# Kernel tuning notes

Measured on AMD Instinct MI355X. Metric: run time of the kernel, lower is better.

## Reference

```python
import jax, jax.numpy as jnp
import numpy as np

HEADS = 8
DIM_HEAD = 64
SCALE = DIM_HEAD ** -0.5

def setup_inputs() -> dict:
    key = jax.random.key(0)
    k1, k2, k3 = jax.random.split(key, 3)
    B, N, D = 4, 2048, 512
    inner = HEADS * DIM_HEAD  # 512
    x = jax.random.normal(k1, (B, N, D), dtype=jnp.float32)
    w_qkv = jax.random.normal(k2, (D, inner * 3), dtype=jnp.float32) * (D ** -0.5)
    w_out = jax.random.normal(k3, (inner, D), dtype=jnp.float32) * (inner ** -0.5)
    b_out = jnp.zeros((D,), dtype=jnp.float32)
    return {"x": x, "w_qkv": w_qkv, "w_out": w_out, "b_out": b_out}

def reference(x, w_qkv, w_out, b_out):
    B, N, D = x.shape
    qkv = x @ w_qkv  # [B, N, 3*inner]
    q, k, v = jnp.split(qkv, 3, axis=-1)
    # b n (h d) -> b h n d
    def to_heads(t):
        return t.reshape(B, N, HEADS, DIM_HEAD).transpose(0, 2, 1, 3)
    q, k, v = to_heads(q), to_heads(k), to_heads(v)
    dots = jnp.einsum('bhid,bhjd->bhij', q, k) * SCALE  # [B,H,N,N]
    attn = jax.nn.softmax(dots, axis=-1)
    out = jnp.einsum('bhij,bhjd->bhid', attn, v)  # [B,H,N,Dh]
    out = out.transpose(0, 2, 1, 3).reshape(B, N, HEADS * DIM_HEAD)
    return out @ w_out + b_out
```

## Files before the change

kernel.cpp:

```cpp
#include <hip/hip_runtime.h>
#include <hip/hip_bf16.h>
#include <math.h>
#include <stdint.h>


typedef unsigned short u16;
typedef __attribute__((ext_vector_type(4))) float f32x4;
typedef __attribute__((ext_vector_type(8))) short bf16x8;
typedef __attribute__((ext_vector_type(4))) short s16x4;

#define AS1 __attribute__((address_space(1)))
#define AS3 __attribute__((address_space(3)))
#define MFMA(a, b, c) __builtin_amdgcn_mfma_f32_16x16x32_bf16(a, b, c, 0, 0, 0)
#define QSCALE 0.180336880f

__device__ __forceinline__ u16 f2bf(float f) {
  union { float f; unsigned u; } v; v.f = f;
  unsigned r = v.u + 0x7FFFu + ((v.u >> 16) & 1u);
  return (u16)(r >> 16);
}
__device__ __forceinline__ float bf2f(u16 b) {
  union { unsigned u; float f; } v; v.u = ((unsigned)b) << 16; return v.f;
}
__device__ __forceinline__ void splitbf(float x, u16& hi, u16& lo) {
  hi = f2bf(x); lo = f2bf(x - bf2f(hi));
}
__device__ __forceinline__ void gld16(const u16* g, u16* l) {
  __builtin_amdgcn_global_load_lds((const AS1 void*)g, (AS3 void*)l, 16, 0, 0);
}
__device__ __forceinline__ float u2f(unsigned u) {
  union { unsigned u; float f; } v; v.u = u; return v.f;
}
__device__ __forceinline__ unsigned f2u(float f) {
  union { float f; unsigned u; } v; v.f = f; return v.u;
}
__device__ __forceinline__ int cvtpk(float lo, float hi) {
  int r; asm("v_cvt_pk_bf16_f32 %0, %1, %2" : "=v"(r) : "v"(lo), "v"(hi));
  return r;
}
__device__ __forceinline__ float fexp2(float x) {
  float r; asm("v_exp_f32 %0, %1" : "=v"(r) : "v"(x));
  return r;
}

__global__ void k_cast(const float* __restrict__ s, u16* __restrict__ h, int n) {
  int i = (blockIdx.x * 256 + threadIdx.x) * 4;
  if (i < n) {
    f32x4 v = *(const f32x4*)&s[i];
    s16x4 hh;
    #pragma unroll
    for (int j = 0; j < 4; ++j) hh[j] = (short)f2bf(v[j]);
    *(s16x4*)&h[i] = hh;
  }
}

__global__ void k_tsplit(const float* __restrict__ s, u16* __restrict__ h,
                         u16* __restrict__ l, int N, int total) {
  int i = blockIdx.x * 256 + threadIdx.x;
  if (i < total) {
    int n = i >> 9, k = i & 511;
    u16 a, b; splitbf(s[(size_t)k * N + n], a, b);
    h[i] = a; l[i] = b;
  }
}

template <int TERMS>
__device__ __forceinline__ void gemm_core(
    const u16* __restrict__ Ah,
    const u16* __restrict__ Bh, const u16* __restrict__ Bl,
    char* sm, int rowA, int rowB, int tid, f32x4 (&acc)[4][4]) {
  const int wid = tid >> 6, lane = tid & 63;
  const int x = lane & 15, h = lane >> 4;
  const int wr = wid >> 1, wc = wid & 1;
  const int d0 = wid * 1024 + lane * 16;
  const int lg0 = d0 ^ (((d0 >> 7) & 7) << 4);
  const int srow = lg0 >> 6;
  const int scol = (lg0 & 63) >> 1;
  const int swk = ((lane >> 1) & 7) << 4;
  const char* smA = sm + (((wr * 64 + x) * 64 + h * 16) ^ swk);
  const char* smB = sm + (((wc * 64 + x) * 64 + h * 16) ^ swk);

  for (int kt = 0; kt < 16; ++kt) {
    const int kofs = kt * 32;
    __syncthreads();
    #pragma unroll
    for (int r = 0; r < 2; ++r) {
      const int row  = r * 64 + srow;
      const int ldst = r * 4096 + wid * 1024;
      const size_t ga = (size_t)(rowA + row) * 512 + kofs + scol;
      const size_t gb = (size_t)(rowB + row) * 512 + kofs + scol;
      gld16(Ah + ga, (u16*)(sm + ldst));
      gld16(Bh + gb, (u16*)(sm + 16384 + ldst));
      if (TERMS == 2) gld16(Bl + gb, (u16*)(sm + 24576 + ldst));
    }
    __syncthreads();
    bf16x8 a_h[4], b_h[4], b_l[4];
    #pragma unroll
    for (int i = 0; i < 4; ++i)
      a_h[i] = *(const bf16x8*)(smA + i * 1024);
    #pragma unroll
    for (int j = 0; j < 4; ++j) {
      b_h[j] = *(const bf16x8*)(smB + 16384 + j * 1024);
      if (TERMS == 2) b_l[j] = *(const bf16x8*)(smB + 24576 + j * 1024);
    }
    __builtin_amdgcn_s_setprio(1);
    #pragma unroll
    for (int i = 0; i < 4; ++i)
      #pragma unroll
      for (int j = 0; j < 4; ++j) {
        acc[i][j] = MFMA(a_h[i], b_h[j], acc[i][j]);
        if (TERMS == 2) acc[i][j] = MFMA(a_h[i], b_l[j], acc[i][j]);
      }
    __builtin_amdgcn_s_setprio(0);
  }
}

__global__ __launch_bounds__(256) void k_gemm_qkv(
    const u16* __restrict__ Ah,
    const u16* __restrict__ Bh, const u16* __restrict__ Bl,
    u16* __restrict__ Qb, u16* __restrict__ Kb, u16* __restrict__ Vt) {
  __shared__ __align__(1024) char sm[32768];
  const int tid = threadIdx.x, lane = tid & 63, wid = tid >> 6;
  const int x = lane & 15, h = lane >> 4;
  const int wr = wid >> 1, wc = wid & 1;
  const int rowA = blockIdx.x * 128, rowB = blockIdx.y * 128;
  f32x4 acc[4][4] = {};
  if (rowB >= 1024)
    gemm_core<1>(Ah, Bh, Bl, sm, rowA, rowB, tid, acc);
  else
    gemm_core<2>(Ah, Bh, Bl, sm, rowA, rowB, tid, acc);

  #pragma unroll
  for (int i = 0; i < 4; ++i)
    #pragma unroll
    for (int j = 0; j < 4; ++j) {
      const int n = rowB + wc * 64 + j * 16 + x;
      const int which = n >> 9;
      const int hh = (n >> 6) & 7, d = n & 63;
      const int m0 = rowA + wr * 64 + i * 16 + h * 4;
      const int b = m0 >> 11, is0 = m0 & 2047;
      if (which == 0) {
        #pragma unroll
        for (int r = 0; r < 4; ++r) {
          const size_t idx = ((size_t)((b * 8 + hh) * 2048 + is0 + r)) * 64 + d;
          Qb[idx] = f2bf(acc[i][j][r] * QSCALE);
        }
      } else if (which == 1) {
        #pragma unroll
        for (int r = 0; r < 4; ++r) {
          const size_t idx = ((size_t)((b * 8 + hh) * 2048 + is0 + r)) * 64 + d;
          Kb[idx] = f2bf(acc[i][j][r]);
        }
      } else {
        s16x4 vv;
        #pragma unroll
        for (int r = 0; r < 4; ++r) vv[r] = (short)f2bf(acc[i][j][r]);
        *(s16x4*)&Vt[((size_t)((b * 8 + hh) * 64 + d)) * 2048 + is0] = vv;
      }
    }
}

__global__ __launch_bounds__(256) void k_gemm_out(
    const u16* __restrict__ Ah, const u16* __restrict__ Bh,
    const float* __restrict__ bias, float* __restrict__ out) {
  __shared__ __align__(1024) char sm[32768];
  const int tid = threadIdx.x, lane = tid & 63, wid = tid >> 6;
  const int x = lane & 15, h = lane >> 4;
  const int wr = wid >> 1, wc = wid & 1;
  const int rowA = blockIdx.x * 128, rowB = blockIdx.y * 128;
  f32x4 acc[4][4] = {};
  gemm_core<1>(Ah, Bh, Bh, sm, rowA, rowB, tid, acc);

  #pragma unroll
  for (int i = 0; i < 4; ++i)
    #pragma unroll
    for (int j = 0; j < 4; ++j) {
      const int n = rowB + wc * 64 + j * 16 + x;
      #pragma unroll
      for (int r = 0; r < 4; ++r) {
        const int m = rowA + wr * 64 + i * 16 + h * 4 + r;
        out[(size_t)m * 512 + n] = acc[i][j][r] + bias[n];
      }
    }
}

__global__ __launch_bounds__(128, 2) void k_attn(
    const u16* __restrict__ Qb,
    const u16* __restrict__ Kb, const u16* __restrict__ Vt,
    u16* __restrict__ AO) {
  __shared__ __align__(1024) char sm[40960];
  const int tid = threadIdx.x, wid = tid >> 6, lane = tid & 63;
  const int x = lane & 15, h = lane >> 4;

  const int fid = blockIdx.x;
  const int l = (fid & 7) * 128 + (fid >> 3);
  const int qb = l & 31, bh = l >> 5;

  const size_t base = (size_t)bh * 2048 * 64;
  const int qr0 = qb * 64 + wid * 32;

  bf16x8 qh[2][2];
  #pragma unroll
  for (int g = 0; g < 2; ++g) {
    const size_t rq = base + (size_t)(qr0 + g * 16 + x) * 64 + h * 8;
    #pragma unroll
    for (int ks = 0; ks < 2; ++ks)
      qh[g][ks] = *(const bf16x8*)&Qb[rq + ks * 32];
  }

  bf16x8 ones;
  #pragma unroll
  for (int j = 0; j < 8; ++j) ones[j] = (short)0x3F80;

  int srow[2], scb[2];
  #pragma unroll
  for (int r = 0; r < 2; ++r) {
    const int db = r * 2048 + tid * 16;
    const int lg = db ^ (((db >> 7) & 7) << 4);
    srow[r] = lg >> 6;
    scb[r] = (lg & 63) >> 1;
  }

  const int swk = ((lane >> 1) & 7) << 4;
  const int rdo = (x * 64 + h * 16) ^ swk;
  char* const pb = sm + 32768 + wid * 4096;
  const int pxor = (x & 7) << 4;
  const int prow = x * 128;

  float mrun[2] = {-INFINITY, -INFINITY};
  f32x4 o[2][4] = {};
  f32x4 os[2] = {};

  {
    #pragma unroll
    for (int r = 0; r < 2; ++r) {
      const size_t kR = base + (size_t)srow[r] * 64 + scb[r];
      const size_t vR = base + (size_t)srow[r] * 2048 + scb[r];
      const int db = r * 2048 + tid * 16;
      gld16(Kb + kR,      (u16*)(sm + db));
      gld16(Kb + kR + 32, (u16*)(sm + 4096 + db));
      gld16(Vt + vR,      (u16*)(sm + 8192 + db));
      gld16(Vt + vR + 32, (u16*)(sm + 12288 + db));
    }
  }

  for (int kv = 0; kv < 32; ++kv) {
    const int bb = (kv & 1) * 16384;
    __builtin_amdgcn_s_barrier();
    if (kv < 31) {
      const size_t kvb = (size_t)(kv + 1) * 64;
      char* buf = sm + (16384 - bb);
      #pragma unroll
      for (int r = 0; r < 2; ++r) {
        const size_t kR = base + (kvb + srow[r]) * 64 + scb[r];
        const size_t vR = base + (size_t)srow[r] * 2048 + kvb + scb[r];
        const int db = r * 2048 + tid * 16;
        gld16(Kb + kR,      (u16*)(buf + db));
        gld16(Kb + kR + 32, (u16*)(buf + 4096 + db));
        gld16(Vt + vR,      (u16*)(buf + 8192 + db));
        gld16(Vt + vR + 32, (u16*)(buf + 12288 + db));
      }
      asm volatile("s_waitcnt vmcnt(8)" ::: "memory");
    } else {
      asm volatile("s_waitcnt vmcnt(0)" ::: "memory");
    }
    __builtin_amdgcn_s_barrier();

    const char* smb = sm + bb + rdo;

    f32x4 s[2][4] = {};
    __builtin_amdgcn_s_setprio(1);
    #pragma unroll
    for (int c = 0; c < 4; ++c)
      #pragma unroll
      for (int ks = 0; ks < 2; ++ks) {
        bf16x8 kb_ = *(const bf16x8*)(smb + ks * 4096 + c * 1024);
        s[0][c] = MFMA(kb_, qh[0][ks], s[0][c]);
        s[1][c] = MFMA(kb_, qh[1][ks], s[1][c]);
      }
    __builtin_amdgcn_s_setprio(0);

    float pm[2];
    #pragma unroll
    for (int g = 0; g < 2; ++g) {
      float m0 = fmaxf(fmaxf(s[g][0][0], s[g][0][1]), s[g][0][2]);
      float m1 = fmaxf(fmaxf(s[g][0][3], s[g][1][0]), s[g][1][1]);
      float m2 = fmaxf(fmaxf(s[g][1][2], s[g][1][3]), s[g][2][0]);
      float m3 = fmaxf(fmaxf(s[g][2][1], s[g][2][2]), s[g][2][3]);
      float m4 = fmaxf(fmaxf(s[g][3][0], s[g][3][1]), s[g][3][2]);
      float m5 = fmaxf(fmaxf(m0, m1), m2);
      float p  = fmaxf(fmaxf(fmaxf(m3, m4), s[g][3][3]), m5);
      p = fmaxf(p, __shfl_xor(p, 16, 64));
      p = fmaxf(p, __shfl_xor(p, 32, 64));
      pm[g] = p;
    }

    if (__any((pm[0] > mrun[0] + 7.0f) || (pm[1] > mrun[1] + 7.0f))) {
      #pragma unroll
      for (int g = 0; g < 2; ++g) {
        float mnew = fmaxf(mrun[g], pm[g]);
        float scl = fexp2(mrun[g] - mnew);
        mrun[g] = mnew;
        #pragma unroll
        for (int r = 0; r < 4; ++r) {
          float sq = u2f((unsigned)__builtin_amdgcn_ds_bpermute(
              (20 * h + r) * 4, (int)f2u(scl)));
          os[g][r] *= sq;
          #pragma unroll
          for (int dg = 0; dg < 4; ++dg) o[g][dg][r] *= sq;
        }
      }
    }

    #pragma unroll
    for (int g = 0; g < 2; ++g)
      #pragma unroll
      for (int c = 0; c < 4; ++c) {
        int w0 = cvtpk(fexp2(s[g][c][0] - mrun[g]),
                       fexp2(s[g][c][1] - mrun[g]));
        int w1 = cvtpk(fexp2(s[g][c][2] - mrun[g]),
                       fexp2(s[g][c][3] - mrun[g]));
        int* dst = (int*)(pb + g * 2048 + prow + ((c * 32 + h * 8) ^ pxor));
        dst[0] = w0; dst[1] = w1;
      }

    __builtin_amdgcn_s_setprio(1);
    #pragma unroll
    for (int ch = 0; ch < 2; ++ch) {
      bf16x8 pa0 = *(const bf16x8*)(pb + prow +
                                    ((ch * 64 + h * 16) ^ pxor));
      bf16x8 pa1 = *(const bf16x8*)(pb + 2048 + prow +
                                    ((ch * 64 + h * 16) ^ pxor));
      os[0] = MFMA(pa0, ones, os[0]);
      os[1] = MFMA(pa1, ones, os[1]);
      #pragma unroll
      for (int dg = 0; dg < 4; ++dg) {
        bf16x8 vb = *(const bf16x8*)(smb + 8192 + ch * 4096 + dg * 1024);
        o[0][dg] = MFMA(pa0, vb, o[0][dg]);
        o[1][dg] = MFMA(pa1, vb, o[1][dg]);
      }
    }
    __builtin_amdgcn_s_setprio(0);
  }

  const int b_ = bh >> 3, head = bh & 7;
  #pragma unroll
  for (int g = 0; g < 2; ++g)
    #pragma unroll
    for (int r = 0; r < 4; ++r) {
      const float inv = 1.0f / os[g][r];
      const int row = qr0 + g * 16 + h * 4 + r;
      #pragma unroll
      for (int dg = 0; dg < 4; ++dg) {
        AO[((size_t)(b_ * 2048 + row)) * 512 + head * 64 + dg * 16 + x] =
            f2bf(o[g][dg][r] * inv);
      }
    }
}

extern "C" void kernel_launch(void* const* d_in, const int* in_sizes, int n_in,
                              void* d_out, int out_size, void* d_ws, size_t ws_size,
                              hipStream_t stream) {
  const float* x    = (const float*)d_in[0];
  const float* wqkv = (const float*)d_in[1];
  const float* wout = (const float*)d_in[2];
  const float* bout = (const float*)d_in[3];
  float* out = (float*)d_out;

  char* w = (char*)d_ws;
  u16* xh  = (u16*)(w + 0);
  u16* wqh = (u16*)(w + 16777216);
  u16* wql = (u16*)(w + 18350080);
  u16* woh = (u16*)(w + 19922944);
  u16* wol = (u16*)(w + 20447232);
  u16* Qb  = (u16*)(w + 20971520);
  u16* Kb  = (u16*)(w + 37748736);
  u16* Vt  = (u16*)(w + 46137344);
  u16* AO  = (u16*)(w + 54525952);

  k_cast  <<<4096, 256, 0, stream>>>(x, xh, 4194304);
  k_tsplit<<<3072, 256, 0, stream>>>(wqkv, wqh, wql, 1536, 786432);
  k_tsplit<<<1024, 256, 0, stream>>>(wout, woh, wol, 512, 262144);
  k_gemm_qkv<<<dim3(64, 12), 256, 0, stream>>>(xh, wqh, wql, Qb, Kb, Vt);
  k_attn<<<1024, 128, 0, stream>>>(Qb, Kb, Vt, AO);
  k_gemm_out<<<dim3(64, 4), 256, 0, stream>>>(AO, woh, bout, out);
}
```

Before: 112.1 us.

## Double per-wave query rows in attention kernel to raise K/V reuse

```diff
diff --git a/kernel.cpp b/kernel.cpp
--- a/kernel.cpp
+++ b/kernel.cpp
@@ -188,20 +188,20 @@
     const u16* __restrict__ Qb,
     const u16* __restrict__ Kb, const u16* __restrict__ Vt,
     u16* __restrict__ AO) {
-  __shared__ __align__(1024) char sm[40960];
+  __shared__ __align__(1024) char sm[49152];
   const int tid = threadIdx.x, wid = tid >> 6, lane = tid & 63;
   const int x = lane & 15, h = lane >> 4;
 
   const int fid = blockIdx.x;
-  const int l = (fid & 7) * 128 + (fid >> 3);
-  const int qb = l & 31, bh = l >> 5;
+  const int l = (fid & 7) * 64 + (fid >> 3);
+  const int qb = l & 15, bh = l >> 4;
 
   const size_t base = (size_t)bh * 2048 * 64;
-  const int qr0 = qb * 64 + wid * 32;
-
-  bf16x8 qh[2][2];
-  #pragma unroll
-  for (int g = 0; g < 2; ++g) {
+  const int qr0 = qb * 128 + wid * 64;
+
+  bf16x8 qh[4][2];
+  #pragma unroll
+  for (int g = 0; g < 4; ++g) {
     const size_t rq = base + (size_t)(qr0 + g * 16 + x) * 64 + h * 8;
     #pragma unroll
     for (int ks = 0; ks < 2; ++ks)
@@ -223,13 +223,12 @@
 
   const int swk = ((lane >> 1) & 7) << 4;
   const int rdo = (x * 64 + h * 16) ^ swk;
-  char* const pb = sm + 32768 + wid * 4096;
+  char* const pb = sm + 32768 + wid * 8192;
   const int pxor = (x & 7) << 4;
-  const int prow = x * 128;
-
-  float mrun[2] = {-INFINITY, -INFINITY};
-  f32x4 o[2][4] = {};
-  f32x4 os[2] = {};
+
+  float mrun[4] = {-INFINITY, -INFINITY, -INFINITY, -INFINITY};
+  f32x4 o[4][4] = {};
+  f32x4 os[4] = {};
 
   {
     #pragma unroll
@@ -268,21 +267,22 @@
 
     const char* smb = sm + bb + rdo;
 
-    f32x4 s[2][4] = {};
+    f32x4 s[4][4] = {};
     __builtin_amdgcn_s_setprio(1);
     #pragma unroll
     for (int c = 0; c < 4; ++c)
       #pragma unroll
       for (int ks = 0; ks < 2; ++ks) {
         bf16x8 kb_ = *(const bf16x8*)(smb + ks * 4096 + c * 1024);
-        s[0][c] = MFMA(kb_, qh[0][ks], s[0][c]);
-        s[1][c] = MFMA(kb_, qh[1][ks], s[1][c]);
+        #pragma unroll
+        for (int g = 0; g < 4; ++g)
+          s[g][c] = MFMA(kb_, qh[g][ks], s[g][c]);
       }
     __builtin_amdgcn_s_setprio(0);
 
-    float pm[2];
-    #pragma unroll
-    for (int g = 0; g < 2; ++g) {
+    float pm[4];
+    #pragma unroll
+    for (int g = 0; g < 4; ++g) {
       float m0 = fmaxf(fmaxf(s[g][0][0], s[g][0][1]), s[g][0][2]);
       float m1 = fmaxf(fmaxf(s[g][0][3], s[g][1][0]), s[g][1][1]);
       float m2 = fmaxf(fmaxf(s[g][1][2], s[g][1][3]), s[g][2][0]);
@@ -295,9 +295,10 @@
       pm[g] = p;
     }
 
-    if (__any((pm[0] > mrun[0] + 7.0f) || (pm[1] > mrun[1] + 7.0f))) {
-      #pragma unroll
-      for (int g = 0; g < 2; ++g) {
+    if (__any((pm[0] > mrun[0] + 7.0f) || (pm[1] > mrun[1] + 7.0f) ||
+              (pm[2] > mrun[2] + 7.0f) || (pm[3] > mrun[3] + 7.0f))) {
+      #pragma unroll
+      for (int g = 0; g < 4; ++g) {
         float mnew = fmaxf(mrun[g], pm[g]);
         float scl = fexp2(mrun[g] - mnew);
         mrun[g] = mnew;
@@ -313,31 +314,34 @@
     }
 
     #pragma unroll
-    for (int g = 0; g < 2; ++g)
+    for (int g = 0; g < 4; ++g)
       #pragma unroll
       for (int c = 0; c < 4; ++c) {
         int w0 = cvtpk(fexp2(s[g][c][0] - mrun[g]),
                        fexp2(s[g][c][1] - mrun[g]));
         int w1 = cvtpk(fexp2(s[g][c][2] - mrun[g]),
                        fexp2(s[g][c][3] - mrun[g]));
-        int* dst = (int*)(pb + g * 2048 + prow + ((c * 32 + h * 8) ^ pxor));
+        int* dst = (int*)(pb + (g * 16 + x) * 128 + ((c * 32 + h * 8) ^ pxor));
         dst[0] = w0; dst[1] = w1;
       }
 
     __builtin_amdgcn_s_setprio(1);
     #pragma unroll
     for (int ch = 0; ch < 2; ++ch) {
-      bf16x8 pa0 = *(const bf16x8*)(pb + prow +
-                                    ((ch * 64 + h * 16) ^ pxor));
-      bf16x8 pa1 = *(const bf16x8*)(pb + 2048 + prow +
-                                    ((ch * 64 + h * 16) ^ pxor));
-      os[0] = MFMA(pa0, ones, os[0]);
-      os[1] = MFMA(pa1, ones, os[1]);
+      bf16x8 pa[4];
+      #pragma unroll
+      for (int g = 0; g < 4; ++g)
+        pa[g] = *(const bf16x8*)(pb + (g * 16 + x) * 128 +
+                                 ((ch * 64 + h * 16) ^ pxor));
+      #pragma unroll
+      for (int g = 0; g < 4; ++g)
+        os[g] = MFMA(pa[g], ones, os[g]);
       #pragma unroll
       for (int dg = 0; dg < 4; ++dg) {
         bf16x8 vb = *(const bf16x8*)(smb + 8192 + ch * 4096 + dg * 1024);
-        o[0][dg] = MFMA(pa0, vb, o[0][dg]);
-        o[1][dg] = MFMA(pa1, vb, o[1][dg]);
+        #pragma unroll
+        for (int g = 0; g < 4; ++g)
+          o[g][dg] = MFMA(pa[g], vb, o[g][dg]);
       }
     }
     __builtin_amdgcn_s_setprio(0);
@@ -345,7 +349,7 @@
 
   const int b_ = bh >> 3, head = bh & 7;
   #pragma unroll
-  for (int g = 0; g < 2; ++g)
+  for (int g = 0; g < 4; ++g)
     #pragma unroll
     for (int r = 0; r < 4; ++r) {
       const float inv = 1.0f / os[g][r];
@@ -382,6 +386,6 @@
   k_tsplit<<<3072, 256, 0, stream>>>(wqkv, wqh, wql, 1536, 786432);
   k_tsplit<<<1024, 256, 0, stream>>>(wout, woh, wol, 512, 262144);
   k_gemm_qkv<<<dim3(64, 12), 256, 0, stream>>>(xh, wqh, wql, Qb, Kb, Vt);
-  k_attn<<<1024, 128, 0, stream>>>(Qb, Kb, Vt, AO);
+  k_attn<<<512, 128, 0, stream>>>(Qb, Kb, Vt, AO);
   k_gemm_out<<<dim3(64, 4), 256, 0, stream>>>(AO, woh, bout, out);
 }
```

After: 138.0 us. 1.23x slower.
